# Performance work log

Measured on AMD Instinct MI355X. Metric: run time of the kernel, lower is better.

Reference implementation:

```python
import jax, jax.numpy as jnp
import numpy as np

C = 512   # in_channels
N = 256   # spatial side (H == W required by the bmm structure)


def setup_inputs() -> dict:
    key = jax.random.key(0)
    kx, kf, kg, kh = jax.random.split(key, 4)
    scale = 1.0 / np.sqrt(C)  # spectral-normalized 1x1 conv weights have ~unit spectral norm
    x = jax.random.normal(kx, (C, N, N), dtype=jnp.float32)
    Wf = jax.random.normal(kf, (C, C), dtype=jnp.float32) * scale  # 1x1 conv kernel squeezed
    Wg = jax.random.normal(kg, (C, C), dtype=jnp.float32) * scale
    Wh = jax.random.normal(kh, (C, C), dtype=jnp.float32) * scale
    return {"x": x, "Wf": Wf, "Wg": Wg, "Wh": Wh}


def reference(x, Wf, Wg, Wh):
    # 1x1 convs (no bias) == channel-mixing matmuls: out[c,h,w] = sum_k W[c,k] x[k,h,w]
    f = jnp.einsum('ck,khw->chw', Wf, x)
    g = jnp.einsum('ck,khw->chw', Wg, x)
    h = jnp.einsum('ck,khw->chw', Wh, x)
    # torch.bmm(f, g): per-channel HxW @ HxW matmul -> [C, N, N]
    scores = jnp.einsum('cik,ckj->cij', f, g)
    # nn.Softmax(dim=1) on [C, N, N] -> softmax over the row axis (axis=1)
    attn_map = jax.nn.softmax(scores, axis=1)
    # torch.bmm(h, attn_map) -> [C, N, N]
    attn = jnp.einsum('cik,ckj->cij', h, attn_map)
    return x + attn
```

## Files before the change

kernel.cpp:

```cpp
#include <hip/hip_runtime.h>

typedef unsigned short u16;
typedef unsigned int   u32;
typedef __attribute__((ext_vector_type(8))) _Float16 half8;
typedef __attribute__((ext_vector_type(4))) float f32x4;
typedef __attribute__((ext_vector_type(2))) float f32x2;
typedef __attribute__((ext_vector_type(4))) u32   u32x4;
typedef __attribute__((ext_vector_type(4))) unsigned short u16x4;

#define MFMAH __builtin_amdgcn_mfma_f32_16x16x32_f16

__device__ u16 W16[786432];

__device__ __forceinline__ u16 f2h(float f) {
  _Float16 h = (_Float16)f;
  union { _Float16 hh; u16 u; } cv; cv.hh = h; return cv.u;
}
__device__ __forceinline__ u32 pkh(float a, float b) {
  return (u32)f2h(a) | ((u32)f2h(b) << 16);
}
__device__ __forceinline__ void gload16(const void* g, void* l) {
  __builtin_amdgcn_global_load_lds(
      (const __attribute__((address_space(1))) void*)g,
      (__attribute__((address_space(3))) void*)l, 16, 0, 0);
}

__global__ __launch_bounds__(256)
void prep_w(const float* __restrict__ Wf, const float* __restrict__ Wg,
            const float* __restrict__ Wh)
{
  const int r = blockIdx.x;
  const int k = threadIdx.x * 2;
  const float* src = (r < 512) ? (Wf + (size_t)r * 512)
                   : (r < 1024) ? (Wg + (size_t)(r - 512) * 512)
                                : (Wh + (size_t)(r - 1024) * 512);
  f32x2 v = *(const f32x2*)(src + k);
  *(u32*)(W16 + (size_t)r * 512 + k) = pkh(v[0], v[1]);
}

__global__ __launch_bounds__(256)
void prep_x(const float* __restrict__ x, u16* __restrict__ x16)
{
  __shared__ float tile[64 * 256];
  const int bk = blockIdx.x & 7, bn = blockIdx.x >> 3;
  const int t = threadIdx.x;
  const int cw = (t & 63) * 4, r0 = (t >> 6) * 16;
#pragma unroll
  for (int it = 0; it < 16; ++it) {
    const int r = r0 + it;
    *(f32x4*)&tile[r * 256 + cw] =
        *(const f32x4*)(x + (size_t)(bk * 64 + r) * 65536 + (size_t)bn * 256 + cw);
  }
  __syncthreads();
  u32 w[32];
#pragma unroll
  for (int q = 0; q < 32; ++q)
    w[q] = pkh(tile[(2 * q) * 256 + t], tile[(2 * q + 1) * 256 + t]);
  const size_t ob = (size_t)(bn * 256 + t) * 512 + bk * 64;
#pragma unroll
  for (int c4 = 0; c4 < 8; ++c4)
    *(u32x4*)(x16 + ob + c4 * 8) = (u32x4){w[4*c4], w[4*c4+1], w[4*c4+2], w[4*c4+3]};
}

__global__ __launch_bounds__(256)
void conv_fgh(const u16* __restrict__ x16, u16* __restrict__ fb,
              u16* __restrict__ gTb, u16* __restrict__ hb)
{
  __shared__ u16 sA[8192], sB[8192];
  const int bid = blockIdx.x;
  const int xcd = bid & 7, idx = bid >> 3;
  const int tn = xcd * 64 + idx / 12;
  const int tm = idx % 12;
  const bool gmode = (tm >= 4) && (tm < 8);
  const int t = threadIdx.x, lane = t & 63, wid = t >> 6;
  const int wr = wid >> 1, wc = wid & 1, lr = lane & 15, lq = lane >> 4;

  const int srow = t >> 3, sslot = t & 7;
  int arow_g[4]; size_t bxr_g[4]; int ksw[4];
#pragma unroll
  for (int q = 0; q < 4; ++q) {
    const int row = q * 32 + srow;
    ksw[q] = ((sslot ^ (row & 7)) << 3);
    arow_g[q] = tm * 128 + row;
    const int jg = tn * 128 + row;
    bxr_g[q] = gmode ? ((size_t)(jg & 255) * 256 + (jg >> 8)) : (size_t)jg;
  }

  int offA[4], a7[4], offB[4], b7[4];
#pragma unroll
  for (int mi = 0; mi < 4; ++mi) {
    const int rowA = wr * 64 + mi * 16 + lr;
    offA[mi] = rowA * 64; a7[mi] = rowA & 7;
  }
#pragma unroll
  for (int ni = 0; ni < 4; ++ni) {
    const int rowB = wc * 64 + ni * 16 + lr;
    offB[ni] = rowB * 64; b7[ni] = rowB & 7;
  }

  f32x4 acc[4][4] = {};

  for (int k0 = 0; k0 < 512; k0 += 64) {
#pragma unroll
    for (int q = 0; q < 4; ++q) {
      gload16(W16 + (size_t)arow_g[q] * 512 + k0 + ksw[q], (char*)sA + q * 4096 + t * 16);
      gload16(x16 + bxr_g[q] * 512 + k0 + ksw[q],          (char*)sB + q * 4096 + t * 16);
    }
    __syncthreads();
#pragma unroll
    for (int kk = 0; kk < 2; ++kk) {
      half8 a[4], b[4];
#pragma unroll
      for (int mi = 0; mi < 4; ++mi)
        a[mi] = *(const half8*)(sA + offA[mi] + (((kk * 4 + lq) ^ a7[mi]) << 3));
#pragma unroll
      for (int ni = 0; ni < 4; ++ni)
        b[ni] = *(const half8*)(sB + offB[ni] + (((kk * 4 + lq) ^ b7[ni]) << 3));
#pragma unroll
      for (int mi = 0; mi < 4; ++mi)
#pragma unroll
        for (int ni = 0; ni < 4; ++ni)
          acc[mi][ni] = MFMAH(a[mi], b[ni], acc[mi][ni], 0, 0, 0);
    }
    __syncthreads();
  }

  const int cls = tm >> 2;
  u16* dst = (cls == 0) ? fb : (cls == 1) ? gTb : hb;
  const int rbase = (tm & 3) * 128 + wr * 64;
  const int cbase = tn * 128 + wc * 64;
#pragma unroll
  for (int mi = 0; mi < 4; ++mi)
#pragma unroll
    for (int ni = 0; ni < 4; ++ni) {
      const int r0 = rbase + mi * 16 + lq * 4;
      const int cc = cbase + ni * 16 + lr;
#pragma unroll
      for (int r = 0; r < 4; ++r)
        dst[(size_t)(r0 + r) * 65536 + cc] = f2h(acc[mi][ni][r]);
    }
}

__global__ __launch_bounds__(512)
void scores_kernel(const u16* __restrict__ fb, const u16* __restrict__ gTb,
                   u16* __restrict__ Pt)
{
  __shared__ u16 sA[8192];
  __shared__ u16 sB[4096];
  __shared__ float cmax[512], csum[512];
  const int bid = blockIdx.x;
  const int xcd = bid & 7, i2 = bid >> 3;
  const int c = xcd * 64 + (i2 >> 1), jt = i2 & 1;
  const size_t cb = (size_t)c * 65536;
  const int t = threadIdx.x, lane = t & 63, wid = t >> 6;
  const int wr = wid >> 1, wc = wid & 1, lr = lane & 15, lq = lane >> 4;

  const int arow0 = t >> 2, arow1 = 128 + (t >> 2);
  const int aks0 = (((t & 3) ^ ((arow0 >> 1) & 3)) << 3);
  const int aks1 = (((t & 3) ^ ((arow1 >> 1) & 3)) << 3);
  const int brow = t >> 2;
  const int bks  = (((t & 3) ^ ((brow >> 1) & 3)) << 3);

  int offA[4], offB[4];
#pragma unroll
  for (int mi = 0; mi < 4; ++mi) {
    const int rowA = wr * 64 + mi * 16 + lr;
    offA[mi] = rowA * 32 + ((lq ^ ((rowA >> 1) & 3)) << 3);
  }
#pragma unroll
  for (int ni = 0; ni < 4; ++ni) {
    const int rowB = wc * 64 + ni * 16 + lr;
    offB[ni] = rowB * 32 + ((lq ^ ((rowB >> 1) & 3)) << 3);
  }

  f32x4 acc[4][4] = {};

  for (int k0 = 0; k0 < 256; k0 += 32) {
    gload16(fb + cb + (size_t)arow0 * 256 + k0 + aks0, (char*)sA + t * 16);
    gload16(fb + cb + (size_t)arow1 * 256 + k0 + aks1, (char*)sA + 8192 + t * 16);
    gload16(gTb + cb + (size_t)(jt * 128 + brow) * 256 + k0 + bks, (char*)sB + t * 16);
    __syncthreads();
    half8 a[4], b[4];
#pragma unroll
    for (int mi = 0; mi < 4; ++mi) a[mi] = *(const half8*)(sA + offA[mi]);
#pragma unroll
    for (int ni = 0; ni < 4; ++ni) b[ni] = *(const half8*)(sB + offB[ni]);
#pragma unroll
    for (int mi = 0; mi < 4; ++mi)
#pragma unroll
      for (int ni = 0; ni < 4; ++ni)
        acc[mi][ni] = MFMAH(a[mi], b[ni], acc[mi][ni], 0, 0, 0);
    __syncthreads();
  }

#pragma unroll
  for (int ni = 0; ni < 4; ++ni) {
    const int col = wc * 64 + ni * 16 + lr;
    float m = -3.4e38f;
#pragma unroll
    for (int mi = 0; mi < 4; ++mi) {
      f32x4 a = acc[mi][ni];
      m = fmaxf(m, fmaxf(fmaxf(a[0], a[1]), fmaxf(a[2], a[3])));
    }
    m = fmaxf(m, __shfl_xor(m, 16));
    m = fmaxf(m, __shfl_xor(m, 32));
    cmax[wr * 128 + col] = m;
  }
  __syncthreads();
#pragma unroll
  for (int ni = 0; ni < 4; ++ni) {
    const int col = wc * 64 + ni * 16 + lr;
    const float M = fmaxf(fmaxf(cmax[col], cmax[128 + col]),
                          fmaxf(cmax[256 + col], cmax[384 + col]));
    float s = 0.f;
#pragma unroll
    for (int mi = 0; mi < 4; ++mi)
#pragma unroll
      for (int r = 0; r < 4; ++r) {
        float e = __expf(acc[mi][ni][r] - M);
        acc[mi][ni][r] = e; s += e;
      }
    s += __shfl_xor(s, 16);
    s += __shfl_xor(s, 32);
    csum[wr * 128 + col] = s;
  }
  __syncthreads();
#pragma unroll
  for (int ni = 0; ni < 4; ++ni) {
    const int col = wc * 64 + ni * 16 + lr;
    const float rs = 1.f / (csum[col] + csum[128 + col] + csum[256 + col] + csum[384 + col]);
    const int j = jt * 128 + col;
#pragma unroll
    for (int mi = 0; mi < 4; ++mi) {
      u16x4 w = { f2h(acc[mi][ni][0] * rs), f2h(acc[mi][ni][1] * rs),
                  f2h(acc[mi][ni][2] * rs), f2h(acc[mi][ni][3] * rs) };
      *(u16x4*)(Pt + cb + (size_t)j * 256 + wr * 64 + mi * 16 + lq * 4) = w;
    }
  }
}

__global__ __launch_bounds__(512, 4)
void attn_kernel(const u16* __restrict__ hb, const u16* __restrict__ Pt,
                 const float* __restrict__ x, float* __restrict__ out)
{
  __shared__ u16 sA[8192], sB[4096];
  const int bid = blockIdx.x;
  const int xcd = bid & 7, i2 = bid >> 3;
  const int c = xcd * 64 + (i2 >> 1), tn = i2 & 1;
  const size_t cb = (size_t)c * 65536;
  const int t = threadIdx.x, lane = t & 63, wid = t >> 6;
  const int wr = wid >> 1, wc = wid & 1, lr = lane & 15, lq = lane >> 4;

  const int ar0 = t >> 2, ar1 = 128 + (t >> 2);
  const int aks0 = (((t & 3) ^ ((ar0 >> 1) & 3)) << 3);
  const int aks1 = (((t & 3) ^ ((ar1 >> 1) & 3)) << 3);
  const int br = t >> 2;
  const int bks = (((t & 3) ^ ((br >> 1) & 3)) << 3);

  int offA[4], offB[4];
#pragma unroll
  for (int mi = 0; mi < 4; ++mi) {
    const int rowA = wr * 64 + mi * 16 + lr;
    offA[mi] = rowA * 32 + ((lq ^ ((rowA >> 1) & 3)) << 3);
  }
#pragma unroll
  for (int ni = 0; ni < 4; ++ni) {
    const int rowB = wc * 64 + ni * 16 + lr;
    offB[ni] = rowB * 32 + ((lq ^ ((rowB >> 1) & 3)) << 3);
  }

  f32x4 acc[4][4] = {};

  for (int k0 = 0; k0 < 256; k0 += 32) {
    gload16(hb + cb + (size_t)ar0 * 256 + k0 + aks0, (char*)sA + t * 16);
    gload16(hb + cb + (size_t)ar1 * 256 + k0 + aks1, (char*)sA + 8192 + t * 16);
    gload16(Pt + cb + (size_t)(tn * 128 + br) * 256 + k0 + bks, (char*)sB + t * 16);
    __syncthreads();
    half8 a[4], b[4];
#pragma unroll
    for (int mi = 0; mi < 4; ++mi) a[mi] = *(const half8*)(sA + offA[mi]);
#pragma unroll
    for (int ni = 0; ni < 4; ++ni) b[ni] = *(const half8*)(sB + offB[ni]);
#pragma unroll
    for (int mi = 0; mi < 4; ++mi)
#pragma unroll
      for (int ni = 0; ni < 4; ++ni)
        acc[mi][ni] = MFMAH(a[mi], b[ni], acc[mi][ni], 0, 0, 0);
    __syncthreads();
  }

  const float* Xc = x + cb;
  float* Oc = out + cb;
  const int rbase = wr * 64;
  const int cbase = tn * 128 + wc * 64;
#pragma unroll
  for (int mi = 0; mi < 4; ++mi)
#pragma unroll
    for (int ni = 0; ni < 4; ++ni) {
      const int r0 = rbase + mi * 16 + lq * 4, cc = cbase + ni * 16 + lr;
#pragma unroll
      for (int r = 0; r < 4; ++r) {
        const size_t idx = (size_t)(r0 + r) * 256 + cc;
        Oc[idx] = Xc[idx] + acc[mi][ni][r];
      }
    }
}

extern "C" void kernel_launch(void* const* d_in, const int* in_sizes, int n_in,
                              void* d_out, int out_size, void* d_ws, size_t ws_size,
                              hipStream_t stream)
{
  (void)in_sizes; (void)n_in; (void)out_size; (void)ws_size;
  const float* x  = (const float*)d_in[0];
  const float* Wf = (const float*)d_in[1];
  const float* Wg = (const float*)d_in[2];
  const float* Wh = (const float*)d_in[3];
  float* out = (float*)d_out;
  char*  ws  = (char*)d_ws;

  u16* x16  = (u16*)ws;
  u16* gT16 = (u16*)(ws + 67108864);
  u16* h16  = (u16*)(ws + 134217728);
  u16* f16  = (u16*)d_out;
  u16* Pt   = x16;

  dim3 blk(256, 1, 1);
  prep_w       <<<dim3(1536, 1, 1), blk, 0, stream>>>(Wf, Wg, Wh);
  prep_x       <<<dim3(2048, 1, 1), blk, 0, stream>>>(x, x16);
  conv_fgh     <<<dim3(6144, 1, 1), blk, 0, stream>>>(x16, f16, gT16, h16);
  scores_kernel<<<dim3(1024, 1, 1), dim3(512, 1, 1), 0, stream>>>(f16, gT16, Pt);
  attn_kernel  <<<dim3(1024, 1, 1), dim3(512, 1, 1), 0, stream>>>(h16, Pt, x, out);
}
```

Before: 357.3 us.

## Fuse scores, softmax and attention bmm into one per-channel kernel with LDS-resident probabilities

Replaces the separate scores and attention kernels with a single kernel that gives each channel one block. That block computes the full 256x256 score tile, applies the column softmax, writes the fp16 probabilities into a swizzled LDS buffer, and then runs the h @ P matmul straight from LDS before adding the residual. This removes the global write and re-read of the probability matrix, drops one kernel launch, and avoids loading f twice per channel. The cost is about 160KB of LDS per block, which allows only one block per CU and reduces latency hiding. It also moves the f buffer into a larger workspace region.

```diff
diff --git a/kernel.cpp b/kernel.cpp
--- a/kernel.cpp
+++ b/kernel.cpp
@@ -141,167 +141,142 @@
     }
 }
 
-__global__ __launch_bounds__(512)
-void scores_kernel(const u16* __restrict__ fb, const u16* __restrict__ gTb,
-                   u16* __restrict__ Pt)
-{
-  __shared__ u16 sA[8192];
-  __shared__ u16 sB[4096];
-  __shared__ float cmax[512], csum[512];
+__global__ __launch_bounds__(512, 2)
+void fused_sa(const u16* __restrict__ fb, const u16* __restrict__ gTb,
+              const u16* __restrict__ hb, const float* __restrict__ x,
+              float* __restrict__ out)
+{
+  __shared__ u16 lds[81920];
+  char* const L = (char*)lds;
+  float* const cmax = (float*)(L + 147456);
+  float* const csum = (float*)(L + 149504);
   const int bid = blockIdx.x;
-  const int xcd = bid & 7, i2 = bid >> 3;
-  const int c = xcd * 64 + (i2 >> 1), jt = i2 & 1;
+  const int c = (bid & 7) * 64 + (bid >> 3);
   const size_t cb = (size_t)c * 65536;
   const int t = threadIdx.x, lane = t & 63, wid = t >> 6;
-  const int wr = wid >> 1, wc = wid & 1, lr = lane & 15, lq = lane >> 4;
-
-  const int arow0 = t >> 2, arow1 = 128 + (t >> 2);
-  const int aks0 = (((t & 3) ^ ((arow0 >> 1) & 3)) << 3);
-  const int aks1 = (((t & 3) ^ ((arow1 >> 1) & 3)) << 3);
-  const int brow = t >> 2;
-  const int bks  = (((t & 3) ^ ((brow >> 1) & 3)) << 3);
-
-  int offA[4], offB[4];
-#pragma unroll
-  for (int mi = 0; mi < 4; ++mi) {
-    const int rowA = wr * 64 + mi * 16 + lr;
-    offA[mi] = rowA * 32 + ((lq ^ ((rowA >> 1) & 3)) << 3);
-  }
+  const int wr = wid >> 2, wc = wid & 3, lr = lane & 15, lq = lane >> 4;
+
+  const int r0s = t >> 2, r1s = 128 + (t >> 2);
+  const int ks0 = (((t & 3) ^ ((r0s >> 1) & 3)) << 3);
+  const int ks1 = (((t & 3) ^ ((r1s >> 1) & 3)) << 3);
+
+  int offA[8];
+#pragma unroll
+  for (int mi = 0; mi < 8; ++mi) {
+    const int rowA = wr * 128 + mi * 16 + lr;
+    offA[mi] = 131072 + rowA * 64 + ((lq ^ ((rowA >> 1) & 3)) << 4);
+  }
+  int offB[4], jcol[4], ej[4];
 #pragma unroll
   for (int ni = 0; ni < 4; ++ni) {
     const int rowB = wc * 64 + ni * 16 + lr;
-    offB[ni] = rowB * 32 + ((lq ^ ((rowB >> 1) & 3)) << 3);
-  }
-
-  f32x4 acc[4][4] = {};
-
+    offB[ni] = 147456 + rowB * 64 + ((lq ^ ((rowB >> 1) & 3)) << 4);
+    jcol[ni] = rowB;
+    ej[ni] = (rowB & 7) << 1;
+  }
+
+  f32x4 acc1[8][4] = {};
   for (int k0 = 0; k0 < 256; k0 += 32) {
-    gload16(fb + cb + (size_t)arow0 * 256 + k0 + aks0, (char*)sA + t * 16);
-    gload16(fb + cb + (size_t)arow1 * 256 + k0 + aks1, (char*)sA + 8192 + t * 16);
-    gload16(gTb + cb + (size_t)(jt * 128 + brow) * 256 + k0 + bks, (char*)sB + t * 16);
-    __syncthreads();
-    half8 a[4], b[4];
-#pragma unroll
-    for (int mi = 0; mi < 4; ++mi) a[mi] = *(const half8*)(sA + offA[mi]);
-#pragma unroll
-    for (int ni = 0; ni < 4; ++ni) b[ni] = *(const half8*)(sB + offB[ni]);
-#pragma unroll
-    for (int mi = 0; mi < 4; ++mi)
+    gload16(fb + cb + (size_t)r0s * 256 + k0 + ks0, L + 131072 + t * 16);
+    gload16(fb + cb + (size_t)r1s * 256 + k0 + ks1, L + 139264 + t * 16);
+    gload16(gTb + cb + (size_t)r0s * 256 + k0 + ks0, L + 147456 + t * 16);
+    gload16(gTb + cb + (size_t)r1s * 256 + k0 + ks1, L + 155648 + t * 16);
+    __syncthreads();
+    half8 b[4];
+#pragma unroll
+    for (int ni = 0; ni < 4; ++ni) b[ni] = *(const half8*)(L + offB[ni]);
+#pragma unroll
+    for (int mi = 0; mi < 8; ++mi) {
+      half8 a = *(const half8*)(L + offA[mi]);
 #pragma unroll
       for (int ni = 0; ni < 4; ++ni)
-        acc[mi][ni] = MFMAH(a[mi], b[ni], acc[mi][ni], 0, 0, 0);
-    __syncthreads();
-  }
-
-#pragma unroll
-  for (int ni = 0; ni < 4; ++ni) {
-    const int col = wc * 64 + ni * 16 + lr;
+        acc1[mi][ni] = MFMAH(a, b[ni], acc1[mi][ni], 0, 0, 0);
+    }
+    __syncthreads();
+  }
+
+#pragma unroll
+  for (int ni = 0; ni < 4; ++ni) {
     float m = -3.4e38f;
 #pragma unroll
-    for (int mi = 0; mi < 4; ++mi) {
-      f32x4 a = acc[mi][ni];
+    for (int mi = 0; mi < 8; ++mi) {
+      f32x4 a = acc1[mi][ni];
       m = fmaxf(m, fmaxf(fmaxf(a[0], a[1]), fmaxf(a[2], a[3])));
     }
     m = fmaxf(m, __shfl_xor(m, 16));
     m = fmaxf(m, __shfl_xor(m, 32));
-    cmax[wr * 128 + col] = m;
-  }
-  __syncthreads();
-#pragma unroll
-  for (int ni = 0; ni < 4; ++ni) {
-    const int col = wc * 64 + ni * 16 + lr;
-    const float M = fmaxf(fmaxf(cmax[col], cmax[128 + col]),
-                          fmaxf(cmax[256 + col], cmax[384 + col]));
+    cmax[wr * 256 + jcol[ni]] = m;
+  }
+  __syncthreads();
+  float rsv[4];
+#pragma unroll
+  for (int ni = 0; ni < 4; ++ni) {
+    const int j = jcol[ni];
+    const float M = fmaxf(cmax[j], cmax[256 + j]);
     float s = 0.f;
 #pragma unroll
-    for (int mi = 0; mi < 4; ++mi)
+    for (int mi = 0; mi < 8; ++mi)
 #pragma unroll
       for (int r = 0; r < 4; ++r) {
-        float e = __expf(acc[mi][ni][r] - M);
-        acc[mi][ni][r] = e; s += e;
+        float e = __expf(acc1[mi][ni][r] - M);
+        acc1[mi][ni][r] = e; s += e;
       }
     s += __shfl_xor(s, 16);
     s += __shfl_xor(s, 32);
-    csum[wr * 128 + col] = s;
-  }
-  __syncthreads();
-#pragma unroll
-  for (int ni = 0; ni < 4; ++ni) {
-    const int col = wc * 64 + ni * 16 + lr;
-    const float rs = 1.f / (csum[col] + csum[128 + col] + csum[256 + col] + csum[384 + col]);
-    const int j = jt * 128 + col;
-#pragma unroll
-    for (int mi = 0; mi < 4; ++mi) {
-      u16x4 w = { f2h(acc[mi][ni][0] * rs), f2h(acc[mi][ni][1] * rs),
-                  f2h(acc[mi][ni][2] * rs), f2h(acc[mi][ni][3] * rs) };
-      *(u16x4*)(Pt + cb + (size_t)j * 256 + wr * 64 + mi * 16 + lq * 4) = w;
-    }
-  }
-}
-
-__global__ __launch_bounds__(512, 4)
-void attn_kernel(const u16* __restrict__ hb, const u16* __restrict__ Pt,
-                 const float* __restrict__ x, float* __restrict__ out)
-{
-  __shared__ u16 sA[8192], sB[4096];
-  const int bid = blockIdx.x;
-  const int xcd = bid & 7, i2 = bid >> 3;
-  const int c = xcd * 64 + (i2 >> 1), tn = i2 & 1;
-  const size_t cb = (size_t)c * 65536;
-  const int t = threadIdx.x, lane = t & 63, wid = t >> 6;
-  const int wr = wid >> 1, wc = wid & 1, lr = lane & 15, lq = lane >> 4;
-
-  const int ar0 = t >> 2, ar1 = 128 + (t >> 2);
-  const int aks0 = (((t & 3) ^ ((ar0 >> 1) & 3)) << 3);
-  const int aks1 = (((t & 3) ^ ((ar1 >> 1) & 3)) << 3);
-  const int br = t >> 2;
-  const int bks = (((t & 3) ^ ((br >> 1) & 3)) << 3);
-
-  int offA[4], offB[4];
-#pragma unroll
-  for (int mi = 0; mi < 4; ++mi) {
-    const int rowA = wr * 64 + mi * 16 + lr;
-    offA[mi] = rowA * 32 + ((lq ^ ((rowA >> 1) & 3)) << 3);
-  }
-#pragma unroll
-  for (int ni = 0; ni < 4; ++ni) {
-    const int rowB = wc * 64 + ni * 16 + lr;
-    offB[ni] = rowB * 32 + ((lq ^ ((rowB >> 1) & 3)) << 3);
-  }
-
-  f32x4 acc[4][4] = {};
-
+    csum[wr * 256 + jcol[ni]] = s;
+  }
+  __syncthreads();
+#pragma unroll
+  for (int ni = 0; ni < 4; ++ni)
+    rsv[ni] = 1.f / (csum[jcol[ni]] + csum[256 + jcol[ni]]);
+  __syncthreads();
+
+#pragma unroll
+  for (int ni = 0; ni < 4; ++ni) {
+    const int jb = jcol[ni] * 512;
+#pragma unroll
+    for (int mi = 0; mi < 8; ++mi) {
+      const int g = wr * 32 + mi * 4 + lq;
+      u16x4 w = { f2h(acc1[mi][ni][0] * rsv[ni]), f2h(acc1[mi][ni][1] * rsv[ni]),
+                  f2h(acc1[mi][ni][2] * rsv[ni]), f2h(acc1[mi][ni][3] * rsv[ni]) };
+      *(u16x4*)(L + jb + ((g ^ ej[ni]) << 3)) = w;
+    }
+  }
+  __syncthreads();
+
+  f32x4 acc2[8][4] = {};
   for (int k0 = 0; k0 < 256; k0 += 32) {
-    gload16(hb + cb + (size_t)ar0 * 256 + k0 + aks0, (char*)sA + t * 16);
-    gload16(hb + cb + (size_t)ar1 * 256 + k0 + aks1, (char*)sA + 8192 + t * 16);
-    gload16(Pt + cb + (size_t)(tn * 128 + br) * 256 + k0 + bks, (char*)sB + t * 16);
-    __syncthreads();
-    half8 a[4], b[4];
-#pragma unroll
-    for (int mi = 0; mi < 4; ++mi) a[mi] = *(const half8*)(sA + offA[mi]);
-#pragma unroll
-    for (int ni = 0; ni < 4; ++ni) b[ni] = *(const half8*)(sB + offB[ni]);
-#pragma unroll
-    for (int mi = 0; mi < 4; ++mi)
+    gload16(hb + cb + (size_t)r0s * 256 + k0 + ks0, L + 131072 + t * 16);
+    gload16(hb + cb + (size_t)r1s * 256 + k0 + ks1, L + 139264 + t * 16);
+    __syncthreads();
+    half8 b2[4];
+#pragma unroll
+    for (int ni = 0; ni < 4; ++ni) {
+      const int g2 = (k0 >> 2) + lq * 2;
+      b2[ni] = *(const half8*)(L + jcol[ni] * 512 + ((g2 ^ ej[ni]) << 3));
+    }
+#pragma unroll
+    for (int mi = 0; mi < 8; ++mi) {
+      half8 a = *(const half8*)(L + offA[mi]);
 #pragma unroll
       for (int ni = 0; ni < 4; ++ni)
-        acc[mi][ni] = MFMAH(a[mi], b[ni], acc[mi][ni], 0, 0, 0);
+        acc2[mi][ni] = MFMAH(a, b2[ni], acc2[mi][ni], 0, 0, 0);
+    }
     __syncthreads();
   }
 
   const float* Xc = x + cb;
   float* Oc = out + cb;
-  const int rbase = wr * 64;
-  const int cbase = tn * 128 + wc * 64;
-#pragma unroll
-  for (int mi = 0; mi < 4; ++mi)
+#pragma unroll
+  for (int mi = 0; mi < 8; ++mi)
 #pragma unroll
     for (int ni = 0; ni < 4; ++ni) {
-      const int r0 = rbase + mi * 16 + lq * 4, cc = cbase + ni * 16 + lr;
+      const int a0 = wr * 128 + mi * 16 + lq * 4;
+      const int j = jcol[ni];
 #pragma unroll
       for (int r = 0; r < 4; ++r) {
-        const size_t idx = (size_t)(r0 + r) * 256 + cc;
-        Oc[idx] = Xc[idx] + acc[mi][ni][r];
+        const size_t idx = (size_t)(a0 + r) * 256 + j;
+        Oc[idx] = Xc[idx] + acc2[mi][ni][r];
       }
     }
 }
@@ -321,13 +296,11 @@
   u16* x16  = (u16*)ws;
   u16* gT16 = (u16*)(ws + 67108864);
   u16* h16  = (u16*)(ws + 134217728);
-  u16* f16  = (u16*)d_out;
-  u16* Pt   = x16;
+  u16* f16  = (u16*)(ws + 201326592);
 
   dim3 blk(256, 1, 1);
-  prep_w       <<<dim3(1536, 1, 1), blk, 0, stream>>>(Wf, Wg, Wh);
-  prep_x       <<<dim3(2048, 1, 1), blk, 0, stream>>>(x, x16);
-  conv_fgh     <<<dim3(6144, 1, 1), blk, 0, stream>>>(x16, f16, gT16, h16);
-  scores_kernel<<<dim3(1024, 1, 1), dim3(512, 1, 1), 0, stream>>>(f16, gT16, Pt);
-  attn_kernel  <<<dim3(1024, 1, 1), dim3(512, 1, 1), 0, stream>>>(h16, Pt, x, out);
-}
+  prep_w  <<<dim3(1536, 1, 1), blk, 0, stream>>>(Wf, Wg, Wh);
+  prep_x  <<<dim3(2048, 1, 1), blk, 0, stream>>>(x, x16);
+  conv_fgh<<<dim3(6144, 1, 1), blk, 0, stream>>>(x16, f16, gT16, h16);
+  fused_sa<<<dim3(512, 1, 1), dim3(512, 1, 1), 0, stream>>>(f16, gT16, h16, x, out);
+}
```

Measured after the change: 360.8 us. Within noise of the previous version (+1.0%).
